# Kernel optimization log

Hardware: AMD Instinct MI355X
Metric: run time of the kernel (lower is better)

## Reference

```python
import jax, jax.numpy as jnp
import numpy as np

N_FFT = 2048
HOP = 441
WIN_SIZE = 7
PAD = WIN_SIZE // 2
NP_WIN = WIN_SIZE * WIN_SIZE
COV_NORM = NP_WIN / (NP_WIN - 1.0)  # sample covariance, skimage default
DATA_RANGE = 2.0  # skimage float dtype_range (-1,1)
C1 = (0.01 * DATA_RANGE) ** 2
C2 = (0.03 * DATA_RANGE) ** 2
EPS = 1e-8

# periodic hann window (librosa fftbins=True)
_HANN = 0.5 - 0.5 * np.cos(2.0 * np.pi * np.arange(N_FFT) / N_FFT)


def wav_to_spectrogram(x):
    # x: [B, C, S] -> magnitude spectrogram [B, C, T, F]
    pad = N_FFT // 2
    xp = jnp.pad(x, ((0, 0), (0, 0), (pad, pad)), mode='reflect')  # torch 'reflect'
    L = xp.shape[-1]
    n_frames = (L - N_FFT) // HOP + 1
    idx = jnp.arange(n_frames)[:, None] * HOP + jnp.arange(N_FFT)[None, :]
    frames = xp[..., idx] * jnp.asarray(_HANN, xp.dtype)  # [B,C,T,N_FFT]
    spec = jnp.fft.rfft(frames, axis=-1)
    mag = jnp.sqrt(jnp.maximum(spec.real ** 2 + spec.imag ** 2, EPS))
    return mag


def _umean_last(x):
    # 1D uniform mean filter (size 7) along last axis, scipy 'reflect' boundary
    xp = jnp.pad(x, [(0, 0)] * (x.ndim - 1) + [(PAD, PAD)], mode='symmetric')
    cs = jnp.cumsum(xp, axis=-1)
    zero = jnp.zeros(cs.shape[:-1] + (1,), cs.dtype)
    cs = jnp.concatenate([zero, cs], axis=-1)
    return (cs[..., WIN_SIZE:] - cs[..., :-WIN_SIZE]) / WIN_SIZE


def umean2d(x):
    # separable 7x7 uniform filter over last two axes
    x = _umean_last(x)
    x = jnp.swapaxes(_umean_last(jnp.swapaxes(x, -1, -2)), -1, -2)
    return x


def ssim_map_mean(X, Y):
    ux, uy = umean2d(X), umean2d(Y)
    uxx, uyy, uxy = umean2d(X * X), umean2d(Y * Y), umean2d(X * Y)
    vx = COV_NORM * (uxx - ux * ux)
    vy = COV_NORM * (uyy - uy * uy)
    vxy = COV_NORM * (uxy - ux * uy)
    S = ((2 * ux * uy + C1) * (2 * vxy + C2)) / ((ux * ux + uy * uy + C1) * (vx + vy + C2))
    # crop pad on each side (skimage) then mean over the spatial map
    return jnp.mean(S[..., PAD:-PAD, PAD:-PAD], axis=(-2, -1))


def setup_inputs() -> dict:
    key = jax.random.key(0)
    k1, k2 = jax.random.split(key)
    B, C, S = 32, 2, 176400
    output = jax.random.normal(k1, (B, C, S), dtype=jnp.float32)
    target = jax.random.normal(k2, (B, C, S), dtype=jnp.float32)
    return {"output": output, "target": target}


def reference(output, target):
    so = wav_to_spectrogram(output)
    st = wav_to_spectrogram(target)
    res = ssim_map_mean(so, st)  # [B, C]
    return res[..., None, None]  # [B, C, 1, 1]
```

## Files before the change

### kernel.cpp

```cpp
#include <hip/hip_runtime.h>
#include <math.h>

#ifndef M_PI
#define M_PI 3.14159265358979323846
#endif

constexpr int S_LEN    = 176400;
constexpr int NFFT     = 2048;
constexpr int NC       = 1024;
constexpr int HOP_     = 441;
constexpr int T_FRAMES = 401;
constexpr int F_BINS   = 1025;
constexpr int F_STRIDE = 1028;
constexpr int N_CH     = 64;
constexpr float EPS_   = 1e-8f;
constexpr float C1_    = 0.0004f;
constexpr float C2_    = 0.0036f;
constexpr float COV_NORM_ = 49.0f / 48.0f;

constexpr int WIN_OFF  = 0;
constexpr int TWG_OFF  = 2048;
constexpr int UTW_OFF  = 3584;
constexpr int SPEC_OFF = 5696;
constexpr int RPB_     = 10;
constexpr int N_CHUNKS = 40;

__device__ __forceinline__ int phys(int i) { return i ^ ((i >> 2) & 15); }

__device__ __forceinline__ float2 cadd(float2 a, float2 b){ return make_float2(a.x+b.x, a.y+b.y); }
__device__ __forceinline__ float2 csub(float2 a, float2 b){ return make_float2(a.x-b.x, a.y-b.y); }
__device__ __forceinline__ float2 cmul(float2 a, float2 b){ return make_float2(a.x*b.x-a.y*b.y, a.x*b.y+a.y*b.x); }

__global__ __launch_bounds__(256) void init_tables_kernel(float* __restrict__ ws, float* __restrict__ out) {
    const int idx = blockIdx.x * 256 + threadIdx.x;
    if (idx < 64) out[idx] = 0.0f;
    if (idx < NFFT) {
        ws[WIN_OFF + idx] = 0.5f - 0.5f * cosf((float)(2.0 * M_PI / NFFT) * (float)idx);
    }
    if (idx < 768) {
        float ang = -2.0f * (float)M_PI * (float)idx / (float)NC;
        float s, c; sincosf(ang, &s, &c);
        ws[TWG_OFF + 2*idx] = c; ws[TWG_OFF + 2*idx+1] = s;
    }
    if (idx < F_BINS) {
        float ang = -(float)M_PI * (float)idx / (float)NC;
        float s, c; sincosf(ang, &s, &c);
        ws[UTW_OFF + 2*idx] = c; ws[UTW_OFF + 2*idx+1] = s;
    }
}

__global__ __launch_bounds__(256, 8) void stft_mag_kernel(
    const float* __restrict__ x0, const float* __restrict__ x1,
    float* __restrict__ ws, int ch0, int nch, int swizzle)
{
    __shared__ float2 bufA[NC];
    __shared__ float2 bufB[NC];

    const int tid = threadIdx.x;

    int ch, which, t;
    if (swizzle) {
        int g = blockIdx.x;
        ch    = ch0 + (g & 7) * 8 + ((g >> 3) & 7);
        which = (g >> 6) & 1;
        t     = g >> 7;
    } else {
        int bx = blockIdx.x;
        which = bx / T_FRAMES;
        t     = bx - which * T_FRAMES;
        ch    = ch0 + blockIdx.y;
    }

    const float* __restrict__ xin = (which ? x1 : x0) + (size_t)ch * S_LEN;
    const float*  __restrict__ win = ws + WIN_OFF;
    const float2* __restrict__ twg = (const float2*)(ws + TWG_OFF);
    const float2* __restrict__ utw = (const float2*)(ws + UTW_OFF);

    const int base = t * HOP_ - NFFT / 2;
    float* bufAf = (float*)bufA;
    #pragma unroll
    for (int k = 0; k < NFFT / 256; ++k) {
        int n = k * 256 + tid;
        int j = base + n;
        j = (j < 0) ? -j : j;
        j = (j >= S_LEN) ? (2 * S_LEN - 2 - j) : j;
        float v = xin[j] * win[n];
        int ci = n >> 1;
        bufAf[2 * phys(ci) + (n & 1)] = v;
    }
    __syncthreads();

    float2* A = bufA;
    float2* B = bufB;
    #pragma unroll
    for (int i = 0; i < 5; ++i) {
        const int s_ = 1 << (2 * i);
        const int q  = tid & (s_ - 1);
        const int ps = tid - q;

        float2 x0c = A[phys(tid)];
        float2 x1c = A[phys(tid + 256)];
        float2 x2c = A[phys(tid + 512)];
        float2 x3c = A[phys(tid + 768)];

        float2 t0 = cadd(x0c, x2c);
        float2 t1 = csub(x0c, x2c);
        float2 t2 = cadd(x1c, x3c);
        float2 t3 = csub(x1c, x3c);

        float2 y0 = cadd(t0, t2);
        float2 y2 = csub(t0, t2);
        float2 y1 = make_float2(t1.x + t3.y, t1.y - t3.x);
        float2 y3 = make_float2(t1.x - t3.y, t1.y + t3.x);

        float2 w1 = twg[ps];
        float2 w2 = twg[2 * ps];
        float2 w3 = twg[3 * ps];

        float2 z1 = cmul(y1, w1);
        float2 z2 = cmul(y2, w2);
        float2 z3 = cmul(y3, w3);

        const int o = q + 4 * ps;
        B[phys(o)]          = y0;
        B[phys(o + s_)]     = z1;
        B[phys(o + 2 * s_)] = z2;
        B[phys(o + 3 * s_)] = z3;
        __syncthreads();
        float2* tmp = A; A = B; B = tmp;
    }

    float* __restrict__ sout =
        ws + SPEC_OFF + ((size_t)which * nch + (size_t)(ch - ch0)) * (size_t)T_FRAMES * F_STRIDE
                      + (size_t)t * F_STRIDE;
    #pragma unroll
    for (int k = 0; k < 5; ++k) {
        int r = k * 256 + tid;
        if (k < 4 || tid == 0) {
            float2 Zr = A[phys(r & (NC - 1))];
            float2 Zn = A[phys((NC - r) & (NC - 1))];
            float Ex = 0.5f * (Zr.x + Zn.x);
            float Ey = 0.5f * (Zr.y - Zn.y);
            float Ox = 0.5f * (Zr.y + Zn.y);
            float Oy = 0.5f * (Zn.x - Zr.x);
            float2 wu = utw[r];
            float Xx = Ex + wu.x * Ox - wu.y * Oy;
            float Xy = Ey + wu.x * Oy + wu.y * Ox;
            sout[r] = sqrtf(fmaxf(Xx * Xx + Xy * Xy, EPS_));
        }
    }
}

__global__ __launch_bounds__(256) void ssim_kernel(
    const float* __restrict__ ws, float* __restrict__ out,
    int ch0, int nch)
{
    __shared__ float csx[1284], csy[1284], csxx[1284], csyy[1284], csxy[1284];
    __shared__ double red[256];

    const int tid = threadIdx.x;
    const int cg  = blockIdx.y;
    const int ch  = ch0 + cg;
    const float* __restrict__ spec = ws + SPEC_OFF;
    const size_t per_ch = (size_t)T_FRAMES * F_STRIDE;
    const float* __restrict__ X = spec + (size_t)cg * per_ch;
    const float* __restrict__ Y = spec + ((size_t)nch + cg) * per_ch;

    const int t_begin = 3 + blockIdx.x * RPB_;
    const int t_end_  = min(t_begin + RPB_, T_FRAMES - 3);

    const int fv = tid << 2;
    const bool last = (tid == 255);
    const float inv49 = 1.0f / 49.0f;
    double acc = 0.0;

    float sx[4] = {0,0,0,0}, sy[4] = {0,0,0,0}, sxx[4] = {0,0,0,0},
          syy[4] = {0,0,0,0}, sxy[4] = {0,0,0,0};
    float s5[5] = {0,0,0,0,0};

    for (int rr = t_begin - 3; rr < t_begin + 3; ++rr) {
        float4 xv = *(const float4*)(X + (size_t)rr * F_STRIDE + fv);
        float4 yv = *(const float4*)(Y + (size_t)rr * F_STRIDE + fv);
        float xa[4] = {xv.x, xv.y, xv.z, xv.w}, ya[4] = {yv.x, yv.y, yv.z, yv.w};
        #pragma unroll
        for (int c = 0; c < 4; ++c) {
            sx[c] += xa[c]; sy[c] += ya[c];
            sxx[c] += xa[c]*xa[c]; syy[c] += ya[c]*ya[c]; sxy[c] += xa[c]*ya[c];
        }
        if (last) {
            float xe = X[(size_t)rr * F_STRIDE + 1024];
            float ye = Y[(size_t)rr * F_STRIDE + 1024];
            s5[0] += xe; s5[1] += ye; s5[2] += xe*xe; s5[3] += ye*ye; s5[4] += xe*ye;
        }
    }

    float4 ax, ay, bx, by; float a5x=0, a5y=0, b5x=0, b5y=0;
    ax = *(const float4*)(X + (size_t)(t_begin + 3) * F_STRIDE + fv);
    ay = *(const float4*)(Y + (size_t)(t_begin + 3) * F_STRIDE + fv);
    bx = *(const float4*)(X + (size_t)(t_begin - 3) * F_STRIDE + fv);
    by = *(const float4*)(Y + (size_t)(t_begin - 3) * F_STRIDE + fv);
    if (last) {
        a5x = X[(size_t)(t_begin + 3) * F_STRIDE + 1024];
        a5y = Y[(size_t)(t_begin + 3) * F_STRIDE + 1024];
        b5x = X[(size_t)(t_begin - 3) * F_STRIDE + 1024];
        b5y = Y[(size_t)(t_begin - 3) * F_STRIDE + 1024];
    }

    const int fo = 3 + (tid << 2);

    for (int t = t_begin; t < t_end_; ++t) {
        {
            float xa[4] = {ax.x, ax.y, ax.z, ax.w}, ya[4] = {ay.x, ay.y, ay.z, ay.w};
            #pragma unroll
            for (int c = 0; c < 4; ++c) {
                sx[c] += xa[c]; sy[c] += ya[c];
                sxx[c] += xa[c]*xa[c]; syy[c] += ya[c]*ya[c]; sxy[c] += xa[c]*ya[c];
                int p = 5 * tid + c;
                csx[p] = sx[c]; csy[p] = sy[c];
                csxx[p] = sxx[c]; csyy[p] = syy[c]; csxy[p] = sxy[c];
            }
            if (last) {
                s5[0] += a5x; s5[1] += a5y; s5[2] += a5x*a5x; s5[3] += a5y*a5y; s5[4] += a5x*a5y;
                csx[1280] = s5[0]; csy[1280] = s5[1];
                csxx[1280] = s5[2]; csyy[1280] = s5[3]; csxy[1280] = s5[4];
            }
        }
        __syncthreads();

        {
            float xa[4] = {bx.x, bx.y, bx.z, bx.w}, ya[4] = {by.x, by.y, by.z, by.w};
            #pragma unroll
            for (int c = 0; c < 4; ++c) {
                sx[c] -= xa[c]; sy[c] -= ya[c];
                sxx[c] -= xa[c]*xa[c]; syy[c] -= ya[c]*ya[c]; sxy[c] -= xa[c]*ya[c];
            }
            if (last) {
                s5[0] -= b5x; s5[1] -= b5y; s5[2] -= b5x*b5x; s5[3] -= b5y*b5y; s5[4] -= b5x*b5y;
            }
        }
        if (t + 1 < t_end_) {
            ax = *(const float4*)(X + (size_t)(t + 4) * F_STRIDE + fv);
            ay = *(const float4*)(Y + (size_t)(t + 4) * F_STRIDE + fv);
            bx = *(const float4*)(X + (size_t)(t - 2) * F_STRIDE + fv);
            by = *(const float4*)(Y + (size_t)(t - 2) * F_STRIDE + fv);
            if (last) {
                a5x = X[(size_t)(t + 4) * F_STRIDE + 1024];
                a5y = Y[(size_t)(t + 4) * F_STRIDE + 1024];
                b5x = X[(size_t)(t - 2) * F_STRIDE + 1024];
                b5y = Y[(size_t)(t - 2) * F_STRIDE + 1024];
            }
        }

        if (tid < 255) {
            float tx[10], ty[10], txx[10], tyy[10], txy[10];
            #pragma unroll
            for (int d = 0; d < 10; ++d) {
                int p = 5 * tid + d + (d >> 2);
                tx[d] = csx[p]; ty[d] = csy[p];
                txx[d] = csxx[p]; tyy[d] = csyy[p]; txy[d] = csxy[p];
            }
            float wx  = tx[0]+tx[1]+tx[2]+tx[3]+tx[4]+tx[5]+tx[6];
            float wy  = ty[0]+ty[1]+ty[2]+ty[3]+ty[4]+ty[5]+ty[6];
            float wxx = txx[0]+txx[1]+txx[2]+txx[3]+txx[4]+txx[5]+txx[6];
            float wyy = tyy[0]+tyy[1]+tyy[2]+tyy[3]+tyy[4]+tyy[5]+tyy[6];
            float wxy = txy[0]+txy[1]+txy[2]+txy[3]+txy[4]+txy[5]+txy[6];
            #pragma unroll
            for (int c = 0; c < 4; ++c) {
                if (fo + c <= 1021) {
                    float ux  = wx * inv49, uy  = wy * inv49;
                    float uxx = wxx * inv49, uyy = wyy * inv49, uxy = wxy * inv49;
                    float vx  = COV_NORM_ * (uxx - ux * ux);
                    float vy  = COV_NORM_ * (uyy - uy * uy);
                    float vxy = COV_NORM_ * (uxy - ux * uy);
                    float Sv = ((2.f * ux * uy + C1_) * (2.f * vxy + C2_)) /
                               ((ux * ux + uy * uy + C1_) * (vx + vy + C2_));
                    acc += (double)Sv;
                }
                if (c < 3) {
                    wx  += tx[c+7]  - tx[c];
                    wy  += ty[c+7]  - ty[c];
                    wxx += txx[c+7] - txx[c];
                    wyy += tyy[c+7] - tyy[c];
                    wxy += txy[c+7] - txy[c];
                }
            }
        }
        __syncthreads();
    }

    red[tid] = acc;
    __syncthreads();
    for (int off = 128; off > 0; off >>= 1) {
        if (tid < off) red[tid] += red[tid + off];
        __syncthreads();
    }
    if (tid == 0) {
        atomicAdd(&out[ch], (float)(red[0] / (395.0 * 1019.0)));
    }
}

extern "C" void kernel_launch(void* const* d_in, const int* in_sizes, int n_in,
                              void* d_out, int out_size, void* d_ws, size_t ws_size,
                              hipStream_t stream) {
    const float* x0 = (const float*)d_in[0];
    const float* x1 = (const float*)d_in[1];
    float* out = (float*)d_out;
    float* ws  = (float*)d_ws;

    const size_t table_bytes  = (size_t)SPEC_OFF * sizeof(float);
    const size_t per_ch_bytes = (size_t)2 * T_FRAMES * F_STRIDE * sizeof(float);
    int G = (int)((ws_size - table_bytes) / per_ch_bytes);
    if (G > N_CH) G = N_CH;
    if (G < 1)    G = 1;

    init_tables_kernel<<<dim3(16), dim3(256), 0, stream>>>(ws, out);

    for (int ch0 = 0; ch0 < N_CH; ch0 += G) {
        const int nch = (N_CH - ch0 < G) ? (N_CH - ch0) : G;

        if (nch == 64) {
            stft_mag_kernel<<<dim3(T_FRAMES * 128), dim3(256), 0, stream>>>(x0, x1, ws, ch0, nch, 1);
        } else {
            stft_mag_kernel<<<dim3(2 * T_FRAMES, nch), dim3(256), 0, stream>>>(x0, x1, ws, ch0, nch, 0);
        }

        dim3 g2(N_CHUNKS, nch);
        ssim_kernel<<<g2, 256, 0, stream>>>(ws, out, ch0, nch);
    }
}
```

Before: 369.2 us.

## Make SSIM column sums wave-local with halos, replacing block barriers

```diff
diff --git a/kernel.cpp b/kernel.cpp
--- a/kernel.cpp
+++ b/kernel.cpp
@@ -25,6 +25,8 @@
 constexpr int RPB_     = 10;
 constexpr int N_CHUNKS = 40;
 
+#define WAVE_SYNC() asm volatile("s_waitcnt lgkmcnt(0)" ::: "memory")
+
 __device__ __forceinline__ int phys(int i) { return i ^ ((i >> 2) & 15); }
 
 __device__ __forceinline__ float2 cadd(float2 a, float2 b){ return make_float2(a.x+b.x, a.y+b.y); }
@@ -81,10 +83,16 @@
     #pragma unroll
     for (int k = 0; k < NFFT / 256; ++k) {
         int n = k * 256 + tid;
-        int j = base + n;
-        j = (j < 0) ? -j : j;
-        j = (j >= S_LEN) ? (2 * S_LEN - 2 - j) : j;
-        float v = xin[j] * win[n];
+        int s0 = base + k * 256;
+        float v;
+        if (s0 >= 0 && s0 + 256 <= S_LEN) {
+            v = xin[s0 + tid] * win[n];
+        } else {
+            int j = s0 + tid;
+            j = (j < 0) ? -j : j;
+            j = (j >= S_LEN) ? (2 * S_LEN - 2 - j) : j;
+            v = xin[j] * win[n];
+        }
         int ci = n >> 1;
         bufAf[2 * phys(ci) + (n & 1)] = v;
     }
@@ -155,10 +163,12 @@
     const float* __restrict__ ws, float* __restrict__ out,
     int ch0, int nch)
 {
-    __shared__ float csx[1284], csy[1284], csxx[1284], csyy[1284], csxy[1284];
+    __shared__ float S[5][4][328];
     __shared__ double red[256];
 
     const int tid = threadIdx.x;
+    const int wv  = tid >> 6;
+    const int l   = tid & 63;
     const int cg  = blockIdx.y;
     const int ch  = ch0 + cg;
     const float* __restrict__ spec = ws + SPEC_OFF;
@@ -169,44 +179,48 @@
     const int t_begin = 3 + blockIdx.x * RPB_;
     const int t_end_  = min(t_begin + RPB_, T_FRAMES - 3);
 
-    const int fv = tid << 2;
-    const bool last = (tid == 255);
+    const int colb = (wv << 8) + (l << 2);
+    const int eI   = l - 58;
+    const int ecol = (wv << 8) + 256 + eI;
+    const bool has_e = (eI >= 0) && (ecol <= 1024);
+    const int ea = 320 + eI + (eI >> 2);
+
     const float inv49 = 1.0f / 49.0f;
     double acc = 0.0;
 
-    float sx[4] = {0,0,0,0}, sy[4] = {0,0,0,0}, sxx[4] = {0,0,0,0},
-          syy[4] = {0,0,0,0}, sxy[4] = {0,0,0,0};
-    float s5[5] = {0,0,0,0,0};
+    float sx[4]={0,0,0,0}, sy[4]={0,0,0,0}, sxx[4]={0,0,0,0},
+          syy[4]={0,0,0,0}, sxy[4]={0,0,0,0};
+    float es[5]={0,0,0,0,0};
 
     for (int rr = t_begin - 3; rr < t_begin + 3; ++rr) {
-        float4 xv = *(const float4*)(X + (size_t)rr * F_STRIDE + fv);
-        float4 yv = *(const float4*)(Y + (size_t)rr * F_STRIDE + fv);
+        float4 xv = *(const float4*)(X + (size_t)rr * F_STRIDE + colb);
+        float4 yv = *(const float4*)(Y + (size_t)rr * F_STRIDE + colb);
         float xa[4] = {xv.x, xv.y, xv.z, xv.w}, ya[4] = {yv.x, yv.y, yv.z, yv.w};
         #pragma unroll
         for (int c = 0; c < 4; ++c) {
             sx[c] += xa[c]; sy[c] += ya[c];
             sxx[c] += xa[c]*xa[c]; syy[c] += ya[c]*ya[c]; sxy[c] += xa[c]*ya[c];
         }
-        if (last) {
-            float xe = X[(size_t)rr * F_STRIDE + 1024];
-            float ye = Y[(size_t)rr * F_STRIDE + 1024];
-            s5[0] += xe; s5[1] += ye; s5[2] += xe*xe; s5[3] += ye*ye; s5[4] += xe*ye;
-        }
-    }
-
-    float4 ax, ay, bx, by; float a5x=0, a5y=0, b5x=0, b5y=0;
-    ax = *(const float4*)(X + (size_t)(t_begin + 3) * F_STRIDE + fv);
-    ay = *(const float4*)(Y + (size_t)(t_begin + 3) * F_STRIDE + fv);
-    bx = *(const float4*)(X + (size_t)(t_begin - 3) * F_STRIDE + fv);
-    by = *(const float4*)(Y + (size_t)(t_begin - 3) * F_STRIDE + fv);
-    if (last) {
-        a5x = X[(size_t)(t_begin + 3) * F_STRIDE + 1024];
-        a5y = Y[(size_t)(t_begin + 3) * F_STRIDE + 1024];
-        b5x = X[(size_t)(t_begin - 3) * F_STRIDE + 1024];
-        b5y = Y[(size_t)(t_begin - 3) * F_STRIDE + 1024];
-    }
-
-    const int fo = 3 + (tid << 2);
+        if (has_e) {
+            float xe = X[(size_t)rr * F_STRIDE + ecol];
+            float ye = Y[(size_t)rr * F_STRIDE + ecol];
+            es[0] += xe; es[1] += ye; es[2] += xe*xe; es[3] += ye*ye; es[4] += xe*ye;
+        }
+    }
+
+    float4 ax, ay, bx, by; float eax=0, eay=0, ebx=0, eby=0;
+    ax = *(const float4*)(X + (size_t)(t_begin + 3) * F_STRIDE + colb);
+    ay = *(const float4*)(Y + (size_t)(t_begin + 3) * F_STRIDE + colb);
+    bx = *(const float4*)(X + (size_t)(t_begin - 3) * F_STRIDE + colb);
+    by = *(const float4*)(Y + (size_t)(t_begin - 3) * F_STRIDE + colb);
+    if (has_e) {
+        eax = X[(size_t)(t_begin + 3) * F_STRIDE + ecol];
+        eay = Y[(size_t)(t_begin + 3) * F_STRIDE + ecol];
+        ebx = X[(size_t)(t_begin - 3) * F_STRIDE + ecol];
+        eby = Y[(size_t)(t_begin - 3) * F_STRIDE + ecol];
+    }
+
+    const int p5 = 5 * l;
 
     for (int t = t_begin; t < t_end_; ++t) {
         {
@@ -215,17 +229,16 @@
             for (int c = 0; c < 4; ++c) {
                 sx[c] += xa[c]; sy[c] += ya[c];
                 sxx[c] += xa[c]*xa[c]; syy[c] += ya[c]*ya[c]; sxy[c] += xa[c]*ya[c];
-                int p = 5 * tid + c;
-                csx[p] = sx[c]; csy[p] = sy[c];
-                csxx[p] = sxx[c]; csyy[p] = syy[c]; csxy[p] = sxy[c];
-            }
-            if (last) {
-                s5[0] += a5x; s5[1] += a5y; s5[2] += a5x*a5x; s5[3] += a5y*a5y; s5[4] += a5x*a5y;
-                csx[1280] = s5[0]; csy[1280] = s5[1];
-                csxx[1280] = s5[2]; csyy[1280] = s5[3]; csxy[1280] = s5[4];
-            }
-        }
-        __syncthreads();
+                S[0][wv][p5+c] = sx[c];  S[1][wv][p5+c] = sy[c];
+                S[2][wv][p5+c] = sxx[c]; S[3][wv][p5+c] = syy[c]; S[4][wv][p5+c] = sxy[c];
+            }
+            if (has_e) {
+                es[0] += eax; es[1] += eay; es[2] += eax*eax; es[3] += eay*eay; es[4] += eax*eay;
+                S[0][wv][ea] = es[0]; S[1][wv][ea] = es[1];
+                S[2][wv][ea] = es[2]; S[3][wv][ea] = es[3]; S[4][wv][ea] = es[4];
+            }
+        }
+        WAVE_SYNC();
 
         {
             float xa[4] = {bx.x, bx.y, bx.z, bx.w}, ya[4] = {by.x, by.y, by.z, by.w};
@@ -234,30 +247,30 @@
                 sx[c] -= xa[c]; sy[c] -= ya[c];
                 sxx[c] -= xa[c]*xa[c]; syy[c] -= ya[c]*ya[c]; sxy[c] -= xa[c]*ya[c];
             }
-            if (last) {
-                s5[0] -= b5x; s5[1] -= b5y; s5[2] -= b5x*b5x; s5[3] -= b5y*b5y; s5[4] -= b5x*b5y;
+            if (has_e) {
+                es[0] -= ebx; es[1] -= eby; es[2] -= ebx*ebx; es[3] -= eby*eby; es[4] -= ebx*eby;
             }
         }
         if (t + 1 < t_end_) {
-            ax = *(const float4*)(X + (size_t)(t + 4) * F_STRIDE + fv);
-            ay = *(const float4*)(Y + (size_t)(t + 4) * F_STRIDE + fv);
-            bx = *(const float4*)(X + (size_t)(t - 2) * F_STRIDE + fv);
-            by = *(const float4*)(Y + (size_t)(t - 2) * F_STRIDE + fv);
-            if (last) {
-                a5x = X[(size_t)(t + 4) * F_STRIDE + 1024];
-                a5y = Y[(size_t)(t + 4) * F_STRIDE + 1024];
-                b5x = X[(size_t)(t - 2) * F_STRIDE + 1024];
-                b5y = Y[(size_t)(t - 2) * F_STRIDE + 1024];
-            }
-        }
-
-        if (tid < 255) {
+            ax = *(const float4*)(X + (size_t)(t + 4) * F_STRIDE + colb);
+            ay = *(const float4*)(Y + (size_t)(t + 4) * F_STRIDE + colb);
+            bx = *(const float4*)(X + (size_t)(t - 2) * F_STRIDE + colb);
+            by = *(const float4*)(Y + (size_t)(t - 2) * F_STRIDE + colb);
+            if (has_e) {
+                eax = X[(size_t)(t + 4) * F_STRIDE + ecol];
+                eay = Y[(size_t)(t + 4) * F_STRIDE + ecol];
+                ebx = X[(size_t)(t - 2) * F_STRIDE + ecol];
+                eby = Y[(size_t)(t - 2) * F_STRIDE + ecol];
+            }
+        }
+
+        {
             float tx[10], ty[10], txx[10], tyy[10], txy[10];
             #pragma unroll
             for (int d = 0; d < 10; ++d) {
-                int p = 5 * tid + d + (d >> 2);
-                tx[d] = csx[p]; ty[d] = csy[p];
-                txx[d] = csxx[p]; tyy[d] = csyy[p]; txy[d] = csxy[p];
+                int q = p5 + d + (d >> 2);
+                tx[d] = S[0][wv][q]; ty[d] = S[1][wv][q];
+                txx[d] = S[2][wv][q]; tyy[d] = S[3][wv][q]; txy[d] = S[4][wv][q];
             }
             float wx  = tx[0]+tx[1]+tx[2]+tx[3]+tx[4]+tx[5]+tx[6];
             float wy  = ty[0]+ty[1]+ty[2]+ty[3]+ty[4]+ty[5]+ty[6];
@@ -266,7 +279,7 @@
             float wxy = txy[0]+txy[1]+txy[2]+txy[3]+txy[4]+txy[5]+txy[6];
             #pragma unroll
             for (int c = 0; c < 4; ++c) {
-                if (fo + c <= 1021) {
+                if (colb + 3 + c <= 1021) {
                     float ux  = wx * inv49, uy  = wy * inv49;
                     float uxx = wxx * inv49, uyy = wyy * inv49, uxy = wxy * inv49;
                     float vx  = COV_NORM_ * (uxx - ux * ux);
@@ -285,7 +298,7 @@
                 }
             }
         }
-        __syncthreads();
+        WAVE_SYNC();
     }
 
     red[tid] = acc;
```

After: 418.0 us. 1.13x slower.
